# Kernel optimization log

Hardware: AMD Instinct MI355X
Metric: run time of the kernel (lower is better)

The kernel has to match this reference:

```python
import jax, jax.numpy as jnp
import numpy as np

# Standard Human3.6M 17-joint skeleton parents; CHILD_JOINTS[j] = children of joint j.
_PARENTS = np.array([-1, 0, 1, 2, 0, 4, 5, 0, 7, 8, 9, 8, 11, 12, 8, 14, 15])
_J = 17

def _child_mean_matrix():
    """[J,J] matrix M s.t. child_feat = M @ x_joints reproduces the per-joint
    child-mean gather loop (identity row for leaf joints)."""
    M = np.zeros((_J, _J), dtype=np.float32)
    for j in range(_J):
        ch = [i for i in range(_J) if _PARENTS[i] == j]
        if ch:
            M[j, ch] = 1.0 / len(ch)
        else:
            M[j, j] = 1.0
    return M

_CHILD_M = _child_mean_matrix()

B, N, J, C = 8, 243, 17, 512
H = 8
D = C // H

def setup_inputs() -> dict:
    key = jax.random.key(0)
    ks = jax.random.split(key, 9)
    s = 0.02
    return {
        "x": jax.random.normal(ks[0], (B, N, J, C), dtype=jnp.float32),
        "W_qkv": jax.random.normal(ks[1], (C, 3 * C), dtype=jnp.float32) * s,
        "b_qkv": jnp.zeros((3 * C,), dtype=jnp.float32),
        "W_q": jax.random.normal(ks[2], (C, C), dtype=jnp.float32) * s,
        "b_q": jnp.zeros((C,), dtype=jnp.float32),
        "W_kv": jax.random.normal(ks[3], (C, 2 * C), dtype=jnp.float32) * s,
        "b_kv": jnp.zeros((2 * C,), dtype=jnp.float32),
        "W_proj": jax.random.normal(ks[4], (C, C), dtype=jnp.float32) * s,
        "b_proj": jnp.zeros((C,), dtype=jnp.float32),
    }

def _attn(q, k, v, scale):
    # q,k,v: [B,J,N,H,D]; attention over temporal axis N per (b,j,h)
    a = jnp.einsum('bjnhd,bjmhd->bjhnm', q, k) * scale
    a = jax.nn.softmax(a, axis=-1)
    return jnp.einsum('bjhnm,bjmhd->bjnhd', a, v)

def reference(x, W_qkv, b_qkv, W_q, b_q, W_kv, b_kv, W_proj, b_proj):
    Bx, Nx, Jx, Cx = x.shape
    scale = 1.0 / jnp.sqrt(jnp.asarray(D, x.dtype))
    Mchild = jnp.asarray(_CHILD_M, x.dtype)

    xt = jnp.transpose(x, (0, 2, 1, 3))  # [B,J,N,C] -> per-(b,j) temporal sequences

    # Temporal self-attention (TSA)
    qkv = (xt @ W_qkv + b_qkv).reshape(Bx, Jx, Nx, 3, H, D)
    q_t, k_t, v_t = qkv[:, :, :, 0], qkv[:, :, :, 1], qkv[:, :, :, 2]
    x_tsa = _attn(q_t, k_t, v_t, scale).reshape(Bx, Jx, Nx, Cx)

    # Hierarchical temporal cross-attention (HTC): K/V from child-joint mean
    child = jnp.einsum('jk,bknc->bjnc', Mchild, xt)  # [B,J,N,C]
    q_h = (xt @ W_q + b_q).reshape(Bx, Jx, Nx, H, D)
    kv = (child @ W_kv + b_kv).reshape(Bx, Jx, Nx, 2, H, D)
    k_h, v_h = kv[:, :, :, 0], kv[:, :, :, 1]
    x_htc = _attn(q_h, k_h, v_h, scale).reshape(Bx, Jx, Nx, Cx)

    # Fuse, project, residual + LayerNorm (no affine; dropout is identity in eval)
    fuse = jnp.transpose(x_tsa + x_htc, (0, 2, 1, 3))  # [B,N,J,C]
    fuse = fuse @ W_proj + b_proj
    y = x + fuse
    mu = jnp.mean(y, axis=-1, keepdims=True)
    var = jnp.var(y, axis=-1, keepdims=True)
    return (y - mu) / jnp.sqrt(var + 1e-5)
```

## Files before the change

### kernel.cpp

```cpp
#include <hip/hip_runtime.h>

typedef unsigned short u16;
typedef unsigned int u32;
typedef __attribute__((ext_vector_type(8))) short bf16x8;
typedef __attribute__((ext_vector_type(8))) u16  u16x8;
typedef __attribute__((ext_vector_type(4))) float f32x4;

#define TOK   33048
#define NSEQ  243
#define TE    16920576u
#define GSTR  15552
#define VTP   256

__device__ __forceinline__ float bf2f(u16 u){
    union { unsigned int i; float f; } v; v.i = ((unsigned int)u) << 16; return v.f;
}
__device__ __forceinline__ u16 f2bf(float f){
    union { float f; unsigned int i; } v; v.f = f;
    unsigned int r = v.i + 0x7fffu + ((v.i >> 16) & 1u);
    return (u16)(r >> 16);
}

__device__ __forceinline__ void gload_lds16(const void* g, void* l){
    __builtin_amdgcn_global_load_lds(
        (const __attribute__((address_space(1))) unsigned int*)g,
        (__attribute__((address_space(3))) unsigned int*)l, 16, 0, 0);
}

__global__ __launch_bounds__(256) void k_cvt_xbf(const float* __restrict__ x, u16* __restrict__ xbf){
    int idx = blockIdx.x*256 + threadIdx.x;
    int t  = idx >> 6;
    int c8 = (idx & 63) << 3;
    unsigned b   = (unsigned)t / 4131u;
    unsigned rem = (unsigned)t % 4131u;
    unsigned j = rem / 243u, n = rem % 243u;
    const float* src = x + ((size_t)(b*243u + n)*17u + j)*512u + c8;
    f32x4 a = *(const f32x4*)src;
    f32x4 c = *(const f32x4*)(src+4);
    u16x8 o;
    #pragma unroll
    for (int e=0;e<4;e++){ o[e]=f2bf(a[e]); o[e+4]=f2bf(c[e]); }
    *(u16x8*)(xbf + (size_t)t*512 + c8) = o;
}

__global__ __launch_bounds__(256) void k_cvt_wcat(const float* __restrict__ Wqkv,
                                                  const float* __restrict__ Wq,
                                                  const float* __restrict__ Wkv,
                                                  u16* __restrict__ WcatT){
    int idx = blockIdx.x*256 + threadIdx.x;
    int k  = idx / 384;
    int c0 = (idx % 384) * 8;
    const float* src;
    if (c0 < 1536)      src = Wqkv + (size_t)k*1536 + c0;
    else if (c0 < 2048) src = Wq   + (size_t)k*512  + (c0 - 1536);
    else                src = Wkv  + (size_t)k*1024 + (c0 - 2048);
    f32x4 a = *(const f32x4*)src;
    f32x4 b = *(const f32x4*)(src+4);
    #pragma unroll
    for (int e=0;e<4;e++){
        WcatT[(size_t)(c0+e)*512 + k]   = f2bf(a[e]);
        WcatT[(size_t)(c0+4+e)*512 + k] = f2bf(b[e]);
    }
}

__global__ __launch_bounds__(256) void k_cvt_wproj(const float* __restrict__ Wp, u16* __restrict__ WpT){
    int idx = blockIdx.x*256 + threadIdx.x;
    int k  = idx / 64;
    int c0 = (idx % 64) * 8;
    f32x4 a = *(const f32x4*)(Wp + (size_t)k*512 + c0);
    f32x4 b = *(const f32x4*)(Wp + (size_t)k*512 + c0 + 4);
    #pragma unroll
    for (int e=0;e<4;e++){
        WpT[(size_t)(c0+e)*512 + k]   = f2bf(a[e]);
        WpT[(size_t)(c0+4+e)*512 + k] = f2bf(b[e]);
    }
}

__global__ __launch_bounds__(256) void k_gemm_in(
    const u16* __restrict__ xbf, const u16* __restrict__ WcatT,
    const float* __restrict__ b_qkv, const float* __restrict__ b_q,
    const float* __restrict__ b_kv, u16* __restrict__ ws3, int c_off)
{
    __shared__ __align__(16) u16 smem[8192];
    u16* As = smem;
    u16* Bs = smem + 4096;

    const int orig = blockIdx.x;
    const int xcd  = orig & 7;
    const int wg   = (xcd < 4 ? xcd*389 : 4*389 + (xcd-4)*388) + (orig >> 3);
    const int nt = wg % 12, mt = wg / 12;

    const int tid = threadIdx.x;
    const int w = tid >> 6, lane = tid & 63;
    const int wm = w >> 1, wn = w & 1;
    const int lg = lane >> 4, li = lane & 15;

    const int srow = w*16 + (lane >> 2);
    const int scol = (lane & 3) * 8;
    const u16* gA0 = xbf   + (size_t)(mt*128 + srow)*512 + scol;
    const u16* gA1 = gA0 + (size_t)64*512;
    const u16* gB0 = WcatT + (size_t)(c_off + nt*128 + srow)*512 + scol;
    const u16* gB1 = gB0 + (size_t)64*512;
    u16* lA0 = As + w*512;           u16* lA1 = As + 2048 + w*512;
    u16* lB0 = Bs + w*512;           u16* lB1 = Bs + 2048 + w*512;

    f32x4 acc[4][4];
    #pragma unroll
    for (int i=0;i<4;i++)
        #pragma unroll
        for (int jj=0;jj<4;jj++){ acc[i][jj][0]=0.f; acc[i][jj][1]=0.f; acc[i][jj][2]=0.f; acc[i][jj][3]=0.f; }

    for (int k0 = 0; k0 < 512; k0 += 32){
        __syncthreads();
        gload_lds16(gA0 + k0, lA0);
        gload_lds16(gA1 + k0, lA1);
        gload_lds16(gB0 + k0, lB0);
        gload_lds16(gB1 + k0, lB1);
        __syncthreads();
        bf16x8 av[4], bv[4];
        #pragma unroll
        for (int mf=0;mf<4;mf++) av[mf] = *(const bf16x8*)&As[(wm*64 + mf*16 + li)*32 + lg*8];
        #pragma unroll
        for (int nf=0;nf<4;nf++) bv[nf] = *(const bf16x8*)&Bs[(wn*64 + nf*16 + li)*32 + lg*8];
        #pragma unroll
        for (int mf=0;mf<4;mf++)
            #pragma unroll
            for (int nf=0;nf<4;nf++)
                acc[mf][nf] = __builtin_amdgcn_mfma_f32_16x16x32_bf16(av[mf], bv[nf], acc[mf][nf], 0, 0, 0);
    }

    float bias[4];
    #pragma unroll
    for (int nf=0;nf<4;nf++){
        const int c = c_off + nt*128 + wn*64 + nf*16 + li;
        bias[nf] = (c < 1536) ? b_qkv[c] : (c < 2048 ? b_q[c-1536] : b_kv[c-2048]);
    }

    u16* L = smem + w*1152;
    const int colbase = nt*128 + wn*64;
    const int slot = colbase >> 9;
    const float osc = (slot == 0) ? 0.125f : 1.0f;
    const int hh   = (colbase >> 6) & 7;
    const int rloc = lane & 15;
    const int cchunk = lane >> 4;
    const int dd = (colbase + cchunk*8) & 63;
    u16* tbase = ws3 + (size_t)slot * TE;
    u16* vt    = ws3 + (size_t)2 * TE;

    #pragma unroll
    for (int mf=0;mf<4;mf++){
        __syncthreads();
        #pragma unroll
        for (int nf=0;nf<4;nf++)
            #pragma unroll
            for (int reg=0;reg<4;reg++)
                L[(lg*4+reg)*72 + nf*16 + li] = f2bf((acc[mf][nf][reg] + bias[nf]) * osc);
        __syncthreads();
        const int rr_base = mt*128 + wm*64 + mf*16;
        if (slot < 2){
            const int rr = rr_base + rloc;
            if (rr < TOK){
                u16x8 v0 = *(const u16x8*)&L[rloc*72 + cchunk*8];
                u16x8 v1 = *(const u16x8*)&L[rloc*72 + 32 + cchunk*8];
                const unsigned bj = (unsigned)rr / 243u;
                const unsigned n  = (unsigned)rr % 243u;
                u16* dst = tbase + ((size_t)(bj*8u + hh)*243u + n)*64u + dd;
                *(u16x8*)dst      = v0;
                *(u16x8*)(dst+32) = v1;
            }
        } else {
            u16 colv[16];
            #pragma unroll
            for (int r=0;r<16;r++) colv[r] = L[r*72 + lane];
            if (rr_base < TOK){
                const unsigned bj0 = (unsigned)rr_base / 243u;
                const unsigned n0  = (unsigned)rr_base % 243u;
                if (n0 <= 227 && rr_base + 15 < TOK){
                    u16x8 vlo, vhi;
                    #pragma unroll
                    for (int e=0;e<8;e++){ vlo[e]=colv[e]; vhi[e]=colv[e+8]; }
                    u16* dst = vt + ((size_t)(bj0*8u + hh)*64u + lane)*VTP + n0;
                    *(u16x8*)dst     = vlo;
                    *(u16x8*)(dst+8) = vhi;
                } else {
                    for (int r=0;r<16;r++){
                        const int rr = rr_base + r;
                        if (rr < TOK){
                            const unsigned bjr = (unsigned)rr / 243u;
                            const unsigned nr  = (unsigned)rr % 243u;
                            vt[((size_t)(bjr*8u + hh)*64u + lane)*VTP + nr] = colv[r];
                        }
                    }
                }
            }
        }
    }
}

__constant__ int g_child[17][3] = {
  {1,4,7},{2,-1,-1},{3,-1,-1},{3,-1,-1},{5,-1,-1},{6,-1,-1},{6,-1,-1},{8,-1,-1},
  {9,11,14},{10,-1,-1},{10,-1,-1},{12,-1,-1},{13,-1,-1},{13,-1,-1},{15,-1,-1},
  {16,-1,-1},{16,-1,-1}};
__constant__ float g_cw[17] = {0.33333333f,1,1,1,1,1,1,1,0.33333333f,1,1,1,1,1,1,1,1};

__global__ __launch_bounds__(256) void k_mixk(const u16* __restrict__ Kraw, u16* __restrict__ Kmix){
    const int c = blockIdx.x*256 + threadIdx.x;
    const int g = c / 1944;
    const int off = (c % 1944) * 8;
    const int bj = g >> 3, h = g & 7;
    const int b_ = bj / 17, j_ = bj % 17;
    const float wgt = g_cw[j_];
    float acc[8];
    #pragma unroll
    for (int e=0;e<8;e++) acc[e]=0.f;
    #pragma unroll
    for (int ci=0;ci<3;ci++){
        const int cj = g_child[j_][ci];
        if (cj >= 0){
            const u16x8 v = *(const u16x8*)(Kraw + (size_t)((b_*17+cj)*8+h)*GSTR + off);
            #pragma unroll
            for (int e=0;e<8;e++) acc[e] += wgt*bf2f(v[e]);
        }
    }
    u16x8 o;
    #pragma unroll
    for (int e=0;e<8;e++) o[e]=f2bf(acc[e]);
    *(u16x8*)(Kmix + (size_t)g*GSTR + off) = o;
}

__global__ __launch_bounds__(256) void k_mixv(const u16* __restrict__ VTraw, u16* __restrict__ VTmix){
    const int c = blockIdx.x*256 + threadIdx.x;
    const int g = c / 2048;
    const int off = (c % 2048) * 8;
    const int bj = g >> 3, h = g & 7;
    const int b_ = bj / 17, j_ = bj % 17;
    const float wgt = g_cw[j_];
    float acc[8];
    #pragma unroll
    for (int e=0;e<8;e++) acc[e]=0.f;
    #pragma unroll
    for (int ci=0;ci<3;ci++){
        const int cj = g_child[j_][ci];
        if (cj >= 0){
            const u16x8 v = *(const u16x8*)(VTraw + (size_t)((b_*17+cj)*8+h)*16384u + off);
            #pragma unroll
            for (int e=0;e<8;e++) acc[e] += wgt*bf2f(v[e]);
        }
    }
    u16x8 o;
    #pragma unroll
    for (int e=0;e<8;e++) o[e]=f2bf(acc[e]);
    *(u16x8*)(VTmix + (size_t)g*16384u + off) = o;
}

__global__ __launch_bounds__(256, 3) void k_attn(
    const u16* __restrict__ Qb, const u16* __restrict__ Kb,
    const u16* __restrict__ VTb, u16* __restrict__ attn, int rmw)
{
    __shared__ __align__(16) u16 smem[8192];
    char* kl = (char*)smem;
    char* vl = (char*)smem + 8192;

    const int orig = blockIdx.x;
    const int xcd  = orig & 7;
    const int lin  = orig >> 3;
    const int p2   = lin & 1;
    const int g    = (lin >> 1)*8 + xcd;
    const int bj = g >> 3, h = g & 7;

    const int tid = threadIdx.x, lane = tid & 63, w = tid >> 6;
    const int lg = lane >> 4, li = lane & 15;

    const int qrowA = p2*128 + w*16;
    const int qrowB = qrowA + 64;
    bf16x8 qA0 = {0,0,0,0,0,0,0,0}, qA1 = qA0, qB0 = qA0, qB1 = qA0;
    {
        const int qrA = qrowA + li;
        const u16* qp = Qb + (size_t)g*GSTR + (size_t)qrA*64;
        qA0 = *(const bf16x8*)(qp + lg*8);
        qA1 = *(const bf16x8*)(qp + 32 + lg*8);
        const int qrB = qrowB + li;
        if (qrB < NSEQ){
            const u16* qp2 = Qb + (size_t)g*GSTR + (size_t)qrB*64;
            qB0 = *(const bf16x8*)(qp2 + lg*8);
            qB1 = *(const bf16x8*)(qp2 + 32 + lg*8);
        }
    }

    const int schx = (lane & 7) ^ (lane >> 3);
    const u16* ksrc = Kb  + (size_t)g*GSTR   + (size_t)(w*16 + (lane>>3))*64  + schx*8;
    const u16* vsrc = VTb + (size_t)g*16384u + (size_t)(w*16 + (lane>>3))*VTP + schx*8;
    char* kdst0 = kl + w*2048;
    char* vdst0 = vl + w*2048;

    const int laneA = li + 32*(lg & 1);
    const int laneB = laneA + 16;
    const bool sel = (lg >> 1) != 0;
    const int x7 = li & 7;

    float sumA = 0.f, sumB = 0.f;
    f32x4 oA[4], oB[4];
    #pragma unroll
    for (int dn=0;dn<4;dn++){
        oA[dn][0]=0.f; oA[dn][1]=0.f; oA[dn][2]=0.f; oA[dn][3]=0.f;
        oB[dn][0]=0.f; oB[dn][1]=0.f; oB[dn][2]=0.f; oB[dn][3]=0.f;
    }

    #pragma unroll
    for (int t=0; t<4; t++){
        __syncthreads();
        gload_lds16(ksrc + (size_t)t*4096,        kdst0);
        gload_lds16(ksrc + (size_t)t*4096 + 512,  kdst0 + 1024);
        gload_lds16(vsrc + t*64,                  vdst0);
        gload_lds16(vsrc + t*64 + 8*VTP,          vdst0 + 1024);
        __syncthreads();

        #pragma unroll
        for (int half=0; half<2; half++){
            u32 lo2A[2], hi2A[2], lo2B[2], hi2B[2];
            #pragma unroll
            for (int t2=0; t2<2; t2++){
                const int nt2l = half*2 + t2;
                const int row  = nt2l*16 + li;
                const bf16x8 kb0 = *(const bf16x8*)(kl + row*128 + (((lg  ) ^ x7)<<4));
                const bf16x8 kb1 = *(const bf16x8*)(kl + row*128 + (((4+lg) ^ x7)<<4));
                f32x4 sA; sA[0]=0.f; sA[1]=0.f; sA[2]=0.f; sA[3]=0.f;
                f32x4 sB = sA;
                sA = __builtin_amdgcn_mfma_f32_16x16x32_bf16(kb0, qA0, sA, 0,0,0);
                sA = __builtin_amdgcn_mfma_f32_16x16x32_bf16(kb1, qA1, sA, 0,0,0);
                sB = __builtin_amdgcn_mfma_f32_16x16x32_bf16(kb0, qB0, sB, 0,0,0);
                sB = __builtin_amdgcn_mfma_f32_16x16x32_bf16(kb1, qB1, sB, 0,0,0);
                if (t == 3 && nt2l == 3){
                    sA[3] = -1e30f; sB[3] = -1e30f;
                    if (lg){ sA[0]=-1e30f; sA[1]=-1e30f; sA[2]=-1e30f;
                             sB[0]=-1e30f; sB[1]=-1e30f; sB[2]=-1e30f; }
                }
                const float a0 = __expf(sA[0]);
                const float a1 = __expf(sA[1]);
                const float a2 = __expf(sA[2]);
                const float a3 = __expf(sA[3]);
                sumA += (a0+a1)+(a2+a3);
                lo2A[t2] = (u32)f2bf(a0) | ((u32)f2bf(a1) << 16);
                hi2A[t2] = (u32)f2bf(a2) | ((u32)f2bf(a3) << 16);
                const float b0 = __expf(sB[0]);
                const float b1 = __expf(sB[1]);
                const float b2 = __expf(sB[2]);
                const float b3 = __expf(sB[3]);
                sumB += (b0+b1)+(b2+b3);
                lo2B[t2] = (u32)f2bf(b0) | ((u32)f2bf(b1) << 16);
                hi2B[t2] = (u32)f2bf(b2) | ((u32)f2bf(b3) << 16);
            }
            bf16x8 paA, paB;
            {
                u32 a0 = __shfl((int)lo2A[0], laneA), a1 = __shfl((int)lo2A[1], laneA);
                u32 b0 = __shfl((int)hi2A[0], laneA), b1 = __shfl((int)hi2A[1], laneA);
                u32 c0 = __shfl((int)lo2A[0], laneB), c1 = __shfl((int)lo2A[1], laneB);
                u32 d0 = __shfl((int)hi2A[0], laneB), d1 = __shfl((int)hi2A[1], laneB);
                union { u32 u[4]; bf16x8 v; } pk;
                pk.u[0] = sel ? a1 : a0;
                pk.u[1] = sel ? b1 : b0;
                pk.u[2] = sel ? c1 : c0;
                pk.u[3] = sel ? d1 : d0;
                paA = pk.v;
            }
            {
                u32 a0 = __shfl((int)lo2B[0], laneA), a1 = __shfl((int)lo2B[1], laneA);
                u32 b0 = __shfl((int)hi2B[0], laneA), b1 = __shfl((int)hi2B[1], laneA);
                u32 c0 = __shfl((int)lo2B[0], laneB), c1 = __shfl((int)lo2B[1], laneB);
                u32 d0 = __shfl((int)hi2B[0], laneB), d1 = __shfl((int)hi2B[1], laneB);
                union { u32 u[4]; bf16x8 v; } pk;
                pk.u[0] = sel ? a1 : a0;
                pk.u[1] = sel ? b1 : b0;
                pk.u[2] = sel ? c1 : c0;
                pk.u[3] = sel ? d1 : d0;
                paB = pk.v;
            }
            #pragma unroll
            for (int dn=0;dn<4;dn++){
                const int d = dn*16 + li;
                const bf16x8 vb = *(const bf16x8*)(vl + d*128 + ((((half<<2)+lg) ^ x7)<<4));
                oA[dn] = __builtin_amdgcn_mfma_f32_16x16x32_bf16(paA, vb, oA[dn], 0,0,0);
                oB[dn] = __builtin_amdgcn_mfma_f32_16x16x32_bf16(paB, vb, oB[dn], 0,0,0);
            }
        }
    }

    sumA += __shfl_xor(sumA,16); sumA += __shfl_xor(sumA,32);
    sumB += __shfl_xor(sumB,16); sumB += __shfl_xor(sumB,32);
    const float invA = 1.f/sumA;
    const float invB = 1.f/sumB;
    float invrA[4], invrB[4];
    #pragma unroll
    for (int r=0;r<4;r++){
        invrA[r] = __shfl(invA, lg*4+r);
        invrB[r] = __shfl(invB, lg*4+r);
    }

    #pragma unroll
    for (int dn=0;dn<4;dn++){
        #pragma unroll
        for (int r=0;r<4;r++){
            const int qrow = qrowA + lg*4 + r;
            const size_t off = ((size_t)bj*243 + qrow)*512 + h*64 + dn*16 + li;
            float val = oA[dn][r] * invrA[r];
            if (rmw) val += bf2f(attn[off]);
            attn[off] = f2bf(val);
        }
        #pragma unroll
        for (int r=0;r<4;r++){
            const int qrow = qrowB + lg*4 + r;
            if (qrow < NSEQ){
                const size_t off = ((size_t)bj*243 + qrow)*512 + h*64 + dn*16 + li;
                float val = oB[dn][r] * invrB[r];
                if (rmw) val += bf2f(attn[off]);
                attn[off] = f2bf(val);
            }
        }
    }
}

__global__ __launch_bounds__(256) void k_gemm_proj(
    const u16* __restrict__ attnb, const u16* __restrict__ WprojT,
    const float* __restrict__ b_proj, float* __restrict__ fuse)
{
    __shared__ __align__(16) u16 smem[8192];
    u16* As = smem;
    u16* Bs = smem + 4096;

    const int orig = blockIdx.x;
    const int xcd  = orig & 7;
    const int wg   = (xcd < 4 ? xcd*130 : 4*130 + (xcd-4)*129) + (orig >> 3);
    const int nt = wg & 3, mt = wg >> 2;

    const int tid = threadIdx.x;
    const int w = tid >> 6, lane = tid & 63;
    const int wm = w >> 1, wn = w & 1;
    const int lg = lane >> 4, li = lane & 15;

    const int srow = w*16 + (lane >> 2);
    const int scol = (lane & 3) * 8;
    const u16* gA0 = attnb  + (size_t)(mt*128 + srow)*512 + scol;
    const u16* gA1 = gA0 + (size_t)64*512;
    const u16* gB0 = WprojT + (size_t)(nt*128 + srow)*512 + scol;
    const u16* gB1 = gB0 + (size_t)64*512;
    u16* lA0 = As + w*512;           u16* lA1 = As + 2048 + w*512;
    u16* lB0 = Bs + w*512;           u16* lB1 = Bs + 2048 + w*512;

    f32x4 acc[4][4];
    #pragma unroll
    for (int i=0;i<4;i++)
        #pragma unroll
        for (int jj=0;jj<4;jj++){ acc[i][jj][0]=0.f; acc[i][jj][1]=0.f; acc[i][jj][2]=0.f; acc[i][jj][3]=0.f; }

    for (int k0 = 0; k0 < 512; k0 += 32){
        __syncthreads();
        gload_lds16(gA0 + k0, lA0);
        gload_lds16(gA1 + k0, lA1);
        gload_lds16(gB0 + k0, lB0);
        gload_lds16(gB1 + k0, lB1);
        __syncthreads();
        bf16x8 av[4], bv[4];
        #pragma unroll
        for (int mf=0;mf<4;mf++) av[mf] = *(const bf16x8*)&As[(wm*64 + mf*16 + li)*32 + lg*8];
        #pragma unroll
        for (int nf=0;nf<4;nf++) bv[nf] = *(const bf16x8*)&Bs[(wn*64 + nf*16 + li)*32 + lg*8];
        #pragma unroll
        for (int mf=0;mf<4;mf++)
            #pragma unroll
            for (int nf=0;nf<4;nf++)
                acc[mf][nf] = __builtin_amdgcn_mfma_f32_16x16x32_bf16(av[mf], bv[nf], acc[mf][nf], 0, 0, 0);
    }

    #pragma unroll
    for (int mf=0;mf<4;mf++)
        #pragma unroll
        for (int reg=0;reg<4;reg++){
            const int rr = mt*128 + wm*64 + mf*16 + lg*4 + reg;
            if (rr < TOK){
                #pragma unroll
                for (int nf=0;nf<4;nf++){
                    const int c = nt*128 + wn*64 + nf*16 + li;
                    fuse[(size_t)rr*512 + c] = acc[mf][nf][reg] + b_proj[c];
                }
            }
        }
}

__global__ __launch_bounds__(256) void k_ln(
    const float* __restrict__ x, const float* __restrict__ fuse, float* __restrict__ out)
{
    const int w = threadIdx.x >> 6, lane = threadIdx.x & 63;
    const int o = blockIdx.x*4 + w;
    const unsigned b_  = (unsigned)o / 4131u;
    const unsigned rem = (unsigned)o % 4131u;
    const unsigned n = rem / 17u, j = rem % 17u;
    const unsigned t = (b_*17u + j)*243u + n;
    const float* fr = fuse + (size_t)t*512 + lane*8;
    const float* xr = x    + (size_t)o*512 + lane*8;
    f32x4 f0 = *(const f32x4*)fr, f1 = *(const f32x4*)(fr+4);
    f32x4 x0 = *(const f32x4*)xr, x1 = *(const f32x4*)(xr+4);
    float y[8];
    #pragma unroll
    for (int e=0;e<4;e++){ y[e] = x0[e]+f0[e]; y[e+4] = x1[e]+f1[e]; }
    float s1=0.f, s2=0.f;
    #pragma unroll
    for (int e=0;e<8;e++){ s1 += y[e]; s2 += y[e]*y[e]; }
    #pragma unroll
    for (int m=1;m<64;m<<=1){ s1 += __shfl_xor(s1,m); s2 += __shfl_xor(s2,m); }
    const float mu  = s1 * (1.f/512.f);
    const float var = s2 * (1.f/512.f) - mu*mu;
    const float rstd = rsqrtf(var + 1e-5f);
    float* orow = out + (size_t)o*512 + lane*8;
    f32x4 o0, o1;
    #pragma unroll
    for (int e=0;e<4;e++){ o0[e] = (y[e]-mu)*rstd; o1[e] = (y[e+4]-mu)*rstd; }
    *(f32x4*)orow = o0; *(f32x4*)(orow+4) = o1;
}

extern "C" void kernel_launch(void* const* d_in, const int* in_sizes, int n_in,
                              void* d_out, int out_size, void* d_ws, size_t ws_size,
                              hipStream_t stream)
{
    const float* x      = (const float*)d_in[0];
    const float* W_qkv  = (const float*)d_in[1];
    const float* b_qkv  = (const float*)d_in[2];
    const float* W_q    = (const float*)d_in[3];
    const float* b_q    = (const float*)d_in[4];
    const float* W_kv   = (const float*)d_in[5];
    const float* b_kv   = (const float*)d_in[6];
    const float* W_proj = (const float*)d_in[7];
    const float* b_proj = (const float*)d_in[8];

    char* ws = (char*)d_ws;
    u16*   xbf    = (u16*)(ws);
    u16*   kmix   = (u16*)(ws);
    u16*   ws3    = (u16*)(ws + 33972224u);
    u16*   attn   = (u16*)(ws + 137306112u);
    u16*   WcatT  = (u16*)(ws + 171278336u);
    u16*   WprojT = (u16*)(ws + 174424064u);
    u16*   vtmix  = (u16*)(ws + 174948352u);
    float* fuse   = (float*)(ws + 33972224u);
    float* out    = (float*)d_out;

    k_cvt_xbf  <<<8262, 256, 0, stream>>>(x, xbf);
    k_cvt_wcat <<<768,  256, 0, stream>>>(W_qkv, W_q, W_kv, WcatT);
    k_cvt_wproj<<<128,  256, 0, stream>>>(W_proj, WprojT);

    k_gemm_in<<<3108, 256, 0, stream>>>(xbf, WcatT, b_qkv, b_q, b_kv, ws3, 0);
    k_attn<<<2176, 256, 0, stream>>>(ws3, ws3 + (size_t)TE, ws3 + (size_t)2*TE, attn, 0);

    k_gemm_in<<<3108, 256, 0, stream>>>(xbf, WcatT, b_qkv, b_q, b_kv, ws3, 1536);
    k_mixk<<<8262, 256, 0, stream>>>(ws3 + (size_t)TE, kmix);
    k_mixv<<<8704, 256, 0, stream>>>(ws3 + (size_t)2*TE, vtmix);
    k_attn<<<2176, 256, 0, stream>>>(ws3, kmix, vtmix, attn, 1);

    k_gemm_proj<<<1036, 256, 0, stream>>>(attn, WprojT, b_proj, fuse);

    k_ln<<<8262, 256, 0, stream>>>(x, fuse, out);
}
```

Before: 424.7 us.

## Double-buffer LDS tiles in GEMM and attention kernels to overlap loads

Converts the input GEMM, projection GEMM and attention kernels from single-buffered LDS staging with two barriers per step to a double-buffered scheme. The next K/V or A/B tile is prefetched into the alternate buffer while the current tile is consumed, leaving one barrier per iteration. This aims to hide global-load latency behind MFMA work. It doubles LDS usage per block, which may lower occupancy.

```diff
diff --git a/kernel.cpp b/kernel.cpp
--- a/kernel.cpp
+++ b/kernel.cpp
@@ -81,9 +81,7 @@
     const float* __restrict__ b_qkv, const float* __restrict__ b_q,
     const float* __restrict__ b_kv, u16* __restrict__ ws3, int c_off)
 {
-    __shared__ __align__(16) u16 smem[8192];
-    u16* As = smem;
-    u16* Bs = smem + 4096;
+    __shared__ __align__(16) u16 smem[16384];
 
     const int orig = blockIdx.x;
     const int xcd  = orig & 7;
@@ -101,8 +99,7 @@
     const u16* gA1 = gA0 + (size_t)64*512;
     const u16* gB0 = WcatT + (size_t)(c_off + nt*128 + srow)*512 + scol;
     const u16* gB1 = gB0 + (size_t)64*512;
-    u16* lA0 = As + w*512;           u16* lA1 = As + 2048 + w*512;
-    u16* lB0 = Bs + w*512;           u16* lB1 = Bs + 2048 + w*512;
+    const int ldoff = w*512;
 
     f32x4 acc[4][4];
     #pragma unroll
@@ -110,13 +107,24 @@
         #pragma unroll
         for (int jj=0;jj<4;jj++){ acc[i][jj][0]=0.f; acc[i][jj][1]=0.f; acc[i][jj][2]=0.f; acc[i][jj][3]=0.f; }
 
+    gload_lds16(gA0, smem + ldoff);
+    gload_lds16(gA1, smem + 2048 + ldoff);
+    gload_lds16(gB0, smem + 4096 + ldoff);
+    gload_lds16(gB1, smem + 6144 + ldoff);
+    __syncthreads();
+
+    int cur = 0;
+    #pragma unroll
     for (int k0 = 0; k0 < 512; k0 += 32){
-        __syncthreads();
-        gload_lds16(gA0 + k0, lA0);
-        gload_lds16(gA1 + k0, lA1);
-        gload_lds16(gB0 + k0, lB0);
-        gload_lds16(gB1 + k0, lB1);
-        __syncthreads();
+        if (k0 < 480){
+            u16* nb = smem + (cur^1)*8192;
+            gload_lds16(gA0 + k0 + 32, nb + ldoff);
+            gload_lds16(gA1 + k0 + 32, nb + 2048 + ldoff);
+            gload_lds16(gB0 + k0 + 32, nb + 4096 + ldoff);
+            gload_lds16(gB1 + k0 + 32, nb + 6144 + ldoff);
+        }
+        const u16* As = smem + cur*8192;
+        const u16* Bs = As + 4096;
         bf16x8 av[4], bv[4];
         #pragma unroll
         for (int mf=0;mf<4;mf++) av[mf] = *(const bf16x8*)&As[(wm*64 + mf*16 + li)*32 + lg*8];
@@ -127,6 +135,8 @@
             #pragma unroll
             for (int nf=0;nf<4;nf++)
                 acc[mf][nf] = __builtin_amdgcn_mfma_f32_16x16x32_bf16(av[mf], bv[nf], acc[mf][nf], 0, 0, 0);
+        __syncthreads();
+        cur ^= 1;
     }
 
     float bias[4];
@@ -257,9 +267,7 @@
     const u16* __restrict__ Qb, const u16* __restrict__ Kb,
     const u16* __restrict__ VTb, u16* __restrict__ attn, int rmw)
 {
-    __shared__ __align__(16) u16 smem[8192];
-    char* kl = (char*)smem;
-    char* vl = (char*)smem + 8192;
+    __shared__ __align__(16) u16 smem[16384];
 
     const int orig = blockIdx.x;
     const int xcd  = orig & 7;
@@ -290,8 +298,6 @@
     const int schx = (lane & 7) ^ (lane >> 3);
     const u16* ksrc = Kb  + (size_t)g*GSTR   + (size_t)(w*16 + (lane>>3))*64  + schx*8;
     const u16* vsrc = VTb + (size_t)g*16384u + (size_t)(w*16 + (lane>>3))*VTP + schx*8;
-    char* kdst0 = kl + w*2048;
-    char* vdst0 = vl + w*2048;
 
     const int laneA = li + 32*(lg & 1);
     const int laneB = laneA + 16;
@@ -306,14 +312,27 @@
         oB[dn][0]=0.f; oB[dn][1]=0.f; oB[dn][2]=0.f; oB[dn][3]=0.f;
     }
 
+    {
+        char* b0 = (char*)smem;
+        gload_lds16(ksrc,         b0 + w*2048);
+        gload_lds16(ksrc + 512,   b0 + w*2048 + 1024);
+        gload_lds16(vsrc,         b0 + 8192 + w*2048);
+        gload_lds16(vsrc + 8*VTP, b0 + 8192 + w*2048 + 1024);
+    }
+    __syncthreads();
+
+    int cur = 0;
     #pragma unroll
     for (int t=0; t<4; t++){
-        __syncthreads();
-        gload_lds16(ksrc + (size_t)t*4096,        kdst0);
-        gload_lds16(ksrc + (size_t)t*4096 + 512,  kdst0 + 1024);
-        gload_lds16(vsrc + t*64,                  vdst0);
-        gload_lds16(vsrc + t*64 + 8*VTP,          vdst0 + 1024);
-        __syncthreads();
+        if (t < 3){
+            char* nb = (char*)smem + (cur^1)*16384;
+            gload_lds16(ksrc + (size_t)(t+1)*4096,        nb + w*2048);
+            gload_lds16(ksrc + (size_t)(t+1)*4096 + 512,  nb + w*2048 + 1024);
+            gload_lds16(vsrc + (t+1)*64,                  nb + 8192 + w*2048);
+            gload_lds16(vsrc + (t+1)*64 + 8*VTP,          nb + 8192 + w*2048 + 1024);
+        }
+        char* kl = (char*)smem + cur*16384;
+        char* vl = kl + 8192;
 
         #pragma unroll
         for (int half=0; half<2; half++){
@@ -383,6 +402,8 @@
                 oB[dn] = __builtin_amdgcn_mfma_f32_16x16x32_bf16(paB, vb, oB[dn], 0,0,0);
             }
         }
+        __syncthreads();
+        cur ^= 1;
     }
 
     sumA += __shfl_xor(sumA,16); sumA += __shfl_xor(sumA,32);
@@ -423,9 +444,7 @@
     const u16* __restrict__ attnb, const u16* __restrict__ WprojT,
     const float* __restrict__ b_proj, float* __restrict__ fuse)
 {
-    __shared__ __align__(16) u16 smem[8192];
-    u16* As = smem;
-    u16* Bs = smem + 4096;
+    __shared__ __align__(16) u16 smem[16384];
 
     const int orig = blockIdx.x;
     const int xcd  = orig & 7;
@@ -443,8 +462,7 @@
     const u16* gA1 = gA0 + (size_t)64*512;
     const u16* gB0 = WprojT + (size_t)(nt*128 + srow)*512 + scol;
     const u16* gB1 = gB0 + (size_t)64*512;
-    u16* lA0 = As + w*512;           u16* lA1 = As + 2048 + w*512;
-    u16* lB0 = Bs + w*512;           u16* lB1 = Bs + 2048 + w*512;
+    const int ldoff = w*512;
 
     f32x4 acc[4][4];
     #pragma unroll
@@ -452,13 +470,24 @@
         #pragma unroll
         for (int jj=0;jj<4;jj++){ acc[i][jj][0]=0.f; acc[i][jj][1]=0.f; acc[i][jj][2]=0.f; acc[i][jj][3]=0.f; }
 
+    gload_lds16(gA0, smem + ldoff);
+    gload_lds16(gA1, smem + 2048 + ldoff);
+    gload_lds16(gB0, smem + 4096 + ldoff);
+    gload_lds16(gB1, smem + 6144 + ldoff);
+    __syncthreads();
+
+    int cur = 0;
+    #pragma unroll
     for (int k0 = 0; k0 < 512; k0 += 32){
-        __syncthreads();
-        gload_lds16(gA0 + k0, lA0);
-        gload_lds16(gA1 + k0, lA1);
-        gload_lds16(gB0 + k0, lB0);
-        gload_lds16(gB1 + k0, lB1);
-        __syncthreads();
+        if (k0 < 480){
+            u16* nb = smem + (cur^1)*8192;
+            gload_lds16(gA0 + k0 + 32, nb + ldoff);
+            gload_lds16(gA1 + k0 + 32, nb + 2048 + ldoff);
+            gload_lds16(gB0 + k0 + 32, nb + 4096 + ldoff);
+            gload_lds16(gB1 + k0 + 32, nb + 6144 + ldoff);
+        }
+        const u16* As = smem + cur*8192;
+        const u16* Bs = As + 4096;
         bf16x8 av[4], bv[4];
         #pragma unroll
         for (int mf=0;mf<4;mf++) av[mf] = *(const bf16x8*)&As[(wm*64 + mf*16 + li)*32 + lg*8];
@@ -469,6 +498,8 @@
             #pragma unroll
             for (int nf=0;nf<4;nf++)
                 acc[mf][nf] = __builtin_amdgcn_mfma_f32_16x16x32_bf16(av[mf], bv[nf], acc[mf][nf], 0, 0, 0);
+        __syncthreads();
+        cur ^= 1;
     }
 
     #pragma unroll
```

Result: faster. 383.8 us (-9.6%).
